# Kernel tuning notes

Hardware: AMD Instinct MI355X
Metric: run time of the kernel (lower is better)

The kernel has to match this reference:

```python
import jax, jax.numpy as jnp
import numpy as np

B, H, S, D = 2, 8, 2048, 64
N_HASHES = 6
EPS = 1e-8


def setup_inputs() -> dict:
    key = jax.random.key(0)
    kq, kk, kv, kr = jax.random.split(key, 4)
    Q = jax.random.normal(kq, (B, H, S, D), dtype=jnp.float32)
    K = jax.random.normal(kk, (B, H, S, D), dtype=jnp.float32)
    V = jax.random.normal(kv, (B, H, S, D), dtype=jnp.float32)
    rotations = jax.random.normal(kr, (H, N_HASHES, D), dtype=jnp.float32)
    return {"Q": Q, "K": K, "V": V, "rotations": rotations}


def _buckets(X, rotations, powers):
    # X: [b,h,l,d] -> integer bucket id per position, [b,h,l]
    Xn = X / (jnp.linalg.norm(X, axis=-1, keepdims=True) + 1e-8)
    bits = jnp.einsum('bhld,hnd->bhln', Xn, rotations) > 0
    return jnp.sum(bits.astype(jnp.int32) * powers, axis=-1)


def reference(Q, K, V, rotations):
    n_hashes = rotations.shape[1]
    d = Q.shape[-1]
    powers = (2 ** jnp.arange(n_hashes)).astype(jnp.int32)
    q_buckets = _buckets(Q, rotations, powers)  # [b,h,sq]
    k_buckets = _buckets(K, rotations, powers)  # [b,h,sk]
    # queries only attend to keys whose full hash code matches exactly
    match = q_buckets[..., :, None] == k_buckets[..., None, :]  # [b,h,sq,sk]
    scores = jnp.einsum('bhqd,bhkd->bhqk', Q, K) / (d ** 0.5)
    row_has = jnp.any(match, axis=-1, keepdims=True)
    masked = jnp.where(match, scores, -jnp.inf)
    m = jnp.max(masked, axis=-1, keepdims=True)
    m = jnp.where(row_has, m, 0.0)  # avoid -inf for empty rows
    e = jnp.where(match, jnp.exp(scores - m), 0.0)
    weights = e / (jnp.sum(e, axis=-1, keepdims=True) + EPS)
    out = jnp.einsum('bhqk,bhkd->bhqd', weights, V)
    return out / n_hashes
```

## Files before the change

kernel.cpp:

```cpp
#include <hip/hip_runtime.h>
#include <math.h>


constexpr int S_LEN = 2048;
constexpr int D = 64;
constexpr int NHASH = 6;
constexpr int BH = 16;
constexpr int NB = 64;
constexpr int QPAD = 4;
constexpr int PADQ = S_LEN + (QPAD - 1) * NB;
constexpr int NGRP = PADQ / QPAD;
constexpr int NBLK = NGRP / 4;
constexpr int GSTRIDE = 37;

__global__ __launch_bounds__(256) void lsh_buckets2(const float* __restrict__ Q,
                                                    const float* __restrict__ K,
                                                    const float* __restrict__ rot,
                                                    int* __restrict__ qb,
                                                    int* __restrict__ kb) {
    const int gw   = (blockIdx.x * 256 + threadIdx.x) >> 6;
    const int lane = threadIdx.x & 63;
    const bool isK = gw >= BH * S_LEN;
    const int wid  = isK ? gw - BH * S_LEN : gw;
    const float* X = isK ? K : Q;
    int* dst       = isK ? kb : qb;
    const int h    = (wid >> 11) & 7;

    const float x  = X[(size_t)wid * D + lane];
    const float* r = rot + (size_t)h * NHASH * D + lane;
    float p0 = x * r[0 * D], p1 = x * r[1 * D], p2 = x * r[2 * D];
    float p3 = x * r[3 * D], p4 = x * r[4 * D], p5 = x * r[5 * D];
#pragma unroll
    for (int off = 32; off >= 1; off >>= 1) {
        p0 += __shfl_xor(p0, off, 64);
        p1 += __shfl_xor(p1, off, 64);
        p2 += __shfl_xor(p2, off, 64);
        p3 += __shfl_xor(p3, off, 64);
        p4 += __shfl_xor(p4, off, 64);
        p5 += __shfl_xor(p5, off, 64);
    }
    int bucket = (p0 > 0.f ? 1 : 0) | (p1 > 0.f ? 2 : 0) | (p2 > 0.f ? 4 : 0) |
                 (p3 > 0.f ? 8 : 0) | (p4 > 0.f ? 16 : 0) | (p5 > 0.f ? 32 : 0);
    if (lane == 0) dst[wid] = bucket;
}

__global__ __launch_bounds__(256) void lsh_sortfuse_bh(const int* __restrict__ qbuckets,
                                                       const int* __restrict__ kbuckets,
                                                       int* __restrict__ q_plist,
                                                       int* __restrict__ k_list) {
    __shared__ int hist[NB];
    __shared__ int cur[NB];
    __shared__ int kst[NB], kcnt[NB];
    __shared__ int qst[NB];
    __shared__ int total;
    const int bh  = blockIdx.x;
    const int tid = threadIdx.x;

    if (tid < NB) hist[tid] = 0;
    __syncthreads();
    int myk[8];
#pragma unroll
    for (int i = 0; i < 8; ++i) {
        myk[i] = kbuckets[bh * S_LEN + i * 256 + tid];
        atomicAdd(&hist[myk[i]], 1);
    }
    __syncthreads();
    if (tid < NB) {
        const int cnt = hist[tid];
        int x = cnt;
#pragma unroll
        for (int off = 1; off < 64; off <<= 1) {
            const int y = __shfl_up(x, off, 64);
            if (tid >= off) x += y;
        }
        kst[tid]  = x - cnt;
        kcnt[tid] = cnt;
        cur[tid]  = x - cnt;
    }
    __syncthreads();
    {
        int* klp = k_list + bh * S_LEN;
#pragma unroll
        for (int i = 0; i < 8; ++i) {
            const int b    = myk[i];
            const int slot = atomicAdd(&cur[b], 1);
            klp[slot] = i * 256 + tid;
        }
    }
    __syncthreads();

    if (tid < NB) hist[tid] = 0;
    __syncthreads();
    int myq[8];
#pragma unroll
    for (int i = 0; i < 8; ++i) {
        myq[i] = qbuckets[bh * S_LEN + i * 256 + tid];
        atomicAdd(&hist[myq[i]], 1);
    }
    __syncthreads();
    if (tid < NB) {
        const int cnt = hist[tid];
        const int v   = (cnt + QPAD - 1) & ~(QPAD - 1);
        int x = v;
#pragma unroll
        for (int off = 1; off < 64; off <<= 1) {
            const int y = __shfl_up(x, off, 64);
            if (tid >= off) x += y;
        }
        qst[tid] = x - v;
        cur[tid] = x - v;
        if (tid == 63) total = x;
    }
    __syncthreads();

    int* qp = q_plist + bh * PADQ;
    if (tid < NB) {
        const int cnt    = hist[tid];
        const int padded = (cnt + QPAD - 1) & ~(QPAD - 1);
        const int sent   = 0xFFFF | (kcnt[tid] << 16);
        for (int t = qst[tid] + cnt; t < qst[tid] + padded; ++t) qp[t] = sent;
    }
    for (int t = total + tid; t < PADQ; t += 256) qp[t] = -1;
#pragma unroll
    for (int i = 0; i < 8; ++i) {
        const int b    = myq[i];
        const int slot = atomicAdd(&cur[b], 1);
        const int pos  = slot & 3;
        int e = i * 256 + tid;
        if (pos == 0)      e |= kst[b] << 16;
        else if (pos == 1) e |= kcnt[b] << 16;
        qp[slot] = e;
    }
}

__global__ __launch_bounds__(256) void lsh_attn_g(const float* __restrict__ Q,
                                                  const float* __restrict__ K,
                                                  const float* __restrict__ V,
                                                  const int* __restrict__ q_plist,
                                                  const int* __restrict__ k_list,
                                                  float* __restrict__ out) {
    __shared__ float wbuf[4][QPAD][64];
    __shared__ int   kbuf[4][64];

    const int wv   = threadIdx.x >> 6;
    const int lane = threadIdx.x & 63;
    const int w    = blockIdx.x;
    const int bh   = (w & 7) + 8 * ((w >> 3) & 1);
    const int gb   = ((w >> 4) * GSTRIDE) % NBLK;
    const int grp  = gb * 4 + wv;

    const int* pl = q_plist + bh * PADQ + 4 * grp;
    const int e0 = __builtin_amdgcn_readfirstlane(pl[0]);
    if ((e0 & 0xFFFF) == 0xFFFF) return;
    const int e1 = __builtin_amdgcn_readfirstlane(pl[1]);
    const int e2 = __builtin_amdgcn_readfirstlane(pl[2]);
    const int e3 = __builtin_amdgcn_readfirstlane(pl[3]);

    const int q0 = e0 & 0xFFFF;
    const int ks = (unsigned)e0 >> 16;
    const int nk = (unsigned)e1 >> 16;
    const int t1 = e1 & 0xFFFF, t2 = e2 & 0xFFFF, t3 = e3 & 0xFFFF;
    const bool v1 = t1 != 0xFFFF, v2 = t2 != 0xFFFF, v3 = t3 != 0xFFFF;
    const int q1 = v1 ? t1 : q0;
    const int q2 = v2 ? t2 : q0;
    const int q3 = v3 ? t3 : q0;

    float* outb = out + (size_t)bh * S_LEN * D;
    if (nk == 0) {
        outb[(size_t)q0 * D + lane] = 0.0f;
        if (v1) outb[(size_t)q1 * D + lane] = 0.0f;
        if (v2) outb[(size_t)q2 * D + lane] = 0.0f;
        if (v3) outb[(size_t)q3 * D + lane] = 0.0f;
        return;
    }

    const int* kl     = k_list + bh * S_LEN + ks;
    const float* Kb   = K + (size_t)bh * S_LEN * D;
    const float* Vb   = V + (size_t)bh * S_LEN * D;
    const float* qr0  = Q + ((size_t)bh * S_LEN + q0) * D;
    const float* qr1  = Q + ((size_t)bh * S_LEN + q1) * D;
    const float* qr2  = Q + ((size_t)bh * S_LEN + q2) * D;
    const float* qr3  = Q + ((size_t)bh * S_LEN + q3) * D;

    float l0 = 0.f, l1 = 0.f, l2 = 0.f, l3 = 0.f;
    float acc0 = 0.f, acc1 = 0.f, acc2 = 0.f, acc3 = 0.f;

    for (int c = 0; c * 64 < nk; ++c) {
        const int cnk  = min(64, nk - c * 64);
        const int kidx = kl[c * 64 + min(lane, cnk - 1)];
        const float* krow = Kb + (size_t)kidx * D;

        float s0 = 0.f, s1 = 0.f, s2 = 0.f, s3 = 0.f;
#pragma unroll
        for (int d4 = 0; d4 < 16; ++d4) {
            const float4 kv = *(const float4*)(krow + d4 * 4);
            const float4 a  = *(const float4*)(qr0 + d4 * 4);
            const float4 b  = *(const float4*)(qr1 + d4 * 4);
            const float4 cq = *(const float4*)(qr2 + d4 * 4);
            const float4 dq = *(const float4*)(qr3 + d4 * 4);
            s0 += a.x * kv.x + a.y * kv.y + a.z * kv.z + a.w * kv.w;
            s1 += b.x * kv.x + b.y * kv.y + b.z * kv.z + b.w * kv.w;
            s2 += cq.x * kv.x + cq.y * kv.y + cq.z * kv.z + cq.w * kv.w;
            s3 += dq.x * kv.x + dq.y * kv.y + dq.z * kv.z + dq.w * kv.w;
        }

        const bool kvalid = lane < cnk;
        const float ea = kvalid ? __expf(s0 * 0.125f) : 0.f;
        const float eb = kvalid ? __expf(s1 * 0.125f) : 0.f;
        const float ec = kvalid ? __expf(s2 * 0.125f) : 0.f;
        const float ed = kvalid ? __expf(s3 * 0.125f) : 0.f;
        l0 += ea; l1 += eb; l2 += ec; l3 += ed;
        wbuf[wv][0][lane] = ea;
        wbuf[wv][1][lane] = eb;
        wbuf[wv][2][lane] = ec;
        wbuf[wv][3][lane] = ed;
        kbuf[wv][lane]    = kidx;

        const int ng = (cnk + 3) >> 2;
        for (int g = 0; g < ng; ++g) {
            const int4   kk = *(const int4*)&kbuf[wv][g * 4];
            const float4 eA = *(const float4*)&wbuf[wv][0][g * 4];
            const float4 eB = *(const float4*)&wbuf[wv][1][g * 4];
            const float4 eC = *(const float4*)&wbuf[wv][2][g * 4];
            const float4 eD = *(const float4*)&wbuf[wv][3][g * 4];
            const float vx = Vb[(size_t)kk.x * D + lane];
            const float vy = Vb[(size_t)kk.y * D + lane];
            const float vz = Vb[(size_t)kk.z * D + lane];
            const float vw = Vb[(size_t)kk.w * D + lane];
            acc0 += eA.x * vx + eA.y * vy + eA.z * vz + eA.w * vw;
            acc1 += eB.x * vx + eB.y * vy + eB.z * vz + eB.w * vw;
            acc2 += eC.x * vx + eC.y * vy + eC.z * vz + eC.w * vw;
            acc3 += eD.x * vx + eD.y * vy + eD.z * vz + eD.w * vw;
        }
    }

#pragma unroll
    for (int off = 32; off >= 1; off >>= 1) {
        l0 += __shfl_xor(l0, off, 64);
        l1 += __shfl_xor(l1, off, 64);
        l2 += __shfl_xor(l2, off, 64);
        l3 += __shfl_xor(l3, off, 64);
    }

    const float inv6 = 1.0f / 6.0f;
    outb[(size_t)q0 * D + lane] = acc0 / (l0 + 1e-8f) * inv6;
    if (v1) outb[(size_t)q1 * D + lane] = acc1 / (l1 + 1e-8f) * inv6;
    if (v2) outb[(size_t)q2 * D + lane] = acc2 / (l2 + 1e-8f) * inv6;
    if (v3) outb[(size_t)q3 * D + lane] = acc3 / (l3 + 1e-8f) * inv6;
}

extern "C" void kernel_launch(void* const* d_in, const int* in_sizes, int n_in,
                              void* d_out, int out_size, void* d_ws, size_t ws_size,
                              hipStream_t stream) {
    const float* Q   = (const float*)d_in[0];
    const float* K   = (const float*)d_in[1];
    const float* V   = (const float*)d_in[2];
    const float* rot = (const float*)d_in[3];
    float* out = (float*)d_out;

    char* ws = (char*)d_ws;
    int* q_buckets = (int*)(ws);
    int* k_buckets = (int*)(ws + 131072);
    int* k_list    = (int*)(ws + 262144);
    int* q_plist   = (int*)(ws + 393216);

    lsh_buckets2<<<2 * BH * S_LEN / 4, 256, 0, stream>>>(Q, K, rot, q_buckets, k_buckets);
    lsh_sortfuse_bh<<<BH, 256, 0, stream>>>(q_buckets, k_buckets, q_plist, k_list);
    lsh_attn_g<<<NBLK * BH, 256, 0, stream>>>(Q, K, V, q_plist, k_list, out);
}
```

Before: 75.88 us.

## Pre-pack bucket-sorted K into transposed float4 layout for coalesced score loads

Adds a kernel that gathers K rows in bucket-sorted key order and writes them as [d/4][slot][4] blocks, so the attention kernel reads K with float4 loads that are contiguous across lanes instead of per-lane scattered row reads. The original attention kernel is kept as a fallback when the workspace is too small. The cost is an extra launch plus a full write and re-read of K (about 4 MB).

After: 72.71 us, median of 2. -4.2%, faster.

```diff
diff --git a/kernel.cpp b/kernel.cpp
--- a/kernel.cpp
+++ b/kernel.cpp
@@ -12,6 +12,7 @@
 constexpr int NGRP = PADQ / QPAD;
 constexpr int NBLK = NGRP / 4;
 constexpr int GSTRIDE = 37;
+constexpr size_t KTP_OFF = 1u << 20;
 
 __global__ __launch_bounds__(256) void lsh_buckets2(const float* __restrict__ Q,
                                                     const float* __restrict__ K,
@@ -133,9 +134,29 @@
     }
 }
 
-__global__ __launch_bounds__(256) void lsh_attn_g(const float* __restrict__ Q,
-                                                  const float* __restrict__ K,
+__global__ __launch_bounds__(256) void lsh_kpack(const float* __restrict__ K,
+                                                 const int* __restrict__ k_list,
+                                                 float* __restrict__ Ktp) {
+    const int gw   = (blockIdx.x * 256 + threadIdx.x) >> 6;
+    const int lane = threadIdx.x & 63;
+    const int bh   = gw >> 9;
+    const int s0   = (gw & 511) * 4;
+    const float* Kb = K + (size_t)bh * S_LEN * D;
+    const int* kl   = k_list + bh * S_LEN;
+    float* kt       = Ktp + (size_t)bh * 16 * S_LEN * 4;
+    const int dblk  = lane >> 2, dj = lane & 3;
+#pragma unroll
+    for (int j = 0; j < 4; ++j) {
+        const int slot = s0 + j;
+        const int kidx = kl[slot];
+        const float v  = Kb[(size_t)kidx * D + lane];
+        kt[((size_t)dblk * S_LEN + slot) * 4 + dj] = v;
+    }
+}
+
+__global__ __launch_bounds__(256) void lsh_attn_p(const float* __restrict__ Q,
                                                   const float* __restrict__ V,
+                                                  const float* __restrict__ Ktp,
                                                   const int* __restrict__ q_plist,
                                                   const int* __restrict__ k_list,
                                                   float* __restrict__ out) {
@@ -175,7 +196,7 @@
     }
 
     const int* kl     = k_list + bh * S_LEN + ks;
-    const float* Kb   = K + (size_t)bh * S_LEN * D;
+    const float* ktb  = Ktp + (size_t)bh * 16 * S_LEN * 4;
     const float* Vb   = V + (size_t)bh * S_LEN * D;
     const float* qr0  = Q + ((size_t)bh * S_LEN + q0) * D;
     const float* qr1  = Q + ((size_t)bh * S_LEN + q1) * D;
@@ -187,13 +208,14 @@
 
     for (int c = 0; c * 64 < nk; ++c) {
         const int cnk  = min(64, nk - c * 64);
-        const int kidx = kl[c * 64 + min(lane, cnk - 1)];
-        const float* krow = Kb + (size_t)kidx * D;
+        const int cl   = min(lane, cnk - 1);
+        const int kidx = kl[c * 64 + cl];
+        const int slot = ks + c * 64 + cl;
 
         float s0 = 0.f, s1 = 0.f, s2 = 0.f, s3 = 0.f;
 #pragma unroll
         for (int d4 = 0; d4 < 16; ++d4) {
-            const float4 kv = *(const float4*)(krow + d4 * 4);
+            const float4 kv = *(const float4*)(ktb + ((size_t)d4 * S_LEN + slot) * 4);
             const float4 a  = *(const float4*)(qr0 + d4 * 4);
             const float4 b  = *(const float4*)(qr1 + d4 * 4);
             const float4 cq = *(const float4*)(qr2 + d4 * 4);
@@ -249,6 +271,122 @@
     if (v3) outb[(size_t)q3 * D + lane] = acc3 / (l3 + 1e-8f) * inv6;
 }
 
+__global__ __launch_bounds__(256) void lsh_attn_g(const float* __restrict__ Q,
+                                                  const float* __restrict__ K,
+                                                  const float* __restrict__ V,
+                                                  const int* __restrict__ q_plist,
+                                                  const int* __restrict__ k_list,
+                                                  float* __restrict__ out) {
+    __shared__ float wbuf[4][QPAD][64];
+    __shared__ int   kbuf[4][64];
+
+    const int wv   = threadIdx.x >> 6;
+    const int lane = threadIdx.x & 63;
+    const int w    = blockIdx.x;
+    const int bh   = (w & 7) + 8 * ((w >> 3) & 1);
+    const int gb   = ((w >> 4) * GSTRIDE) % NBLK;
+    const int grp  = gb * 4 + wv;
+
+    const int* pl = q_plist + bh * PADQ + 4 * grp;
+    const int e0 = __builtin_amdgcn_readfirstlane(pl[0]);
+    if ((e0 & 0xFFFF) == 0xFFFF) return;
+    const int e1 = __builtin_amdgcn_readfirstlane(pl[1]);
+    const int e2 = __builtin_amdgcn_readfirstlane(pl[2]);
+    const int e3 = __builtin_amdgcn_readfirstlane(pl[3]);
+
+    const int q0 = e0 & 0xFFFF;
+    const int ks = (unsigned)e0 >> 16;
+    const int nk = (unsigned)e1 >> 16;
+    const int t1 = e1 & 0xFFFF, t2 = e2 & 0xFFFF, t3 = e3 & 0xFFFF;
+    const bool v1 = t1 != 0xFFFF, v2 = t2 != 0xFFFF, v3 = t3 != 0xFFFF;
+    const int q1 = v1 ? t1 : q0;
+    const int q2 = v2 ? t2 : q0;
+    const int q3 = v3 ? t3 : q0;
+
+    float* outb = out + (size_t)bh * S_LEN * D;
+    if (nk == 0) {
+        outb[(size_t)q0 * D + lane] = 0.0f;
+        if (v1) outb[(size_t)q1 * D + lane] = 0.0f;
+        if (v2) outb[(size_t)q2 * D + lane] = 0.0f;
+        if (v3) outb[(size_t)q3 * D + lane] = 0.0f;
+        return;
+    }
+
+    const int* kl     = k_list + bh * S_LEN + ks;
+    const float* Kb   = K + (size_t)bh * S_LEN * D;
+    const float* Vb   = V + (size_t)bh * S_LEN * D;
+    const float* qr0  = Q + ((size_t)bh * S_LEN + q0) * D;
+    const float* qr1  = Q + ((size_t)bh * S_LEN + q1) * D;
+    const float* qr2  = Q + ((size_t)bh * S_LEN + q2) * D;
+    const float* qr3  = Q + ((size_t)bh * S_LEN + q3) * D;
+
+    float l0 = 0.f, l1 = 0.f, l2 = 0.f, l3 = 0.f;
+    float acc0 = 0.f, acc1 = 0.f, acc2 = 0.f, acc3 = 0.f;
+
+    for (int c = 0; c * 64 < nk; ++c) {
+        const int cnk  = min(64, nk - c * 64);
+        const int kidx = kl[c * 64 + min(lane, cnk - 1)];
+        const float* krow = Kb + (size_t)kidx * D;
+
+        float s0 = 0.f, s1 = 0.f, s2 = 0.f, s3 = 0.f;
+#pragma unroll
+        for (int d4 = 0; d4 < 16; ++d4) {
+            const float4 kv = *(const float4*)(krow + d4 * 4);
+            const float4 a  = *(const float4*)(qr0 + d4 * 4);
+            const float4 b  = *(const float4*)(qr1 + d4 * 4);
+            const float4 cq = *(const float4*)(qr2 + d4 * 4);
+            const float4 dq = *(const float4*)(qr3 + d4 * 4);
+            s0 += a.x * kv.x + a.y * kv.y + a.z * kv.z + a.w * kv.w;
+            s1 += b.x * kv.x + b.y * kv.y + b.z * kv.z + b.w * kv.w;
+            s2 += cq.x * kv.x + cq.y * kv.y + cq.z * kv.z + cq.w * kv.w;
+            s3 += dq.x * kv.x + dq.y * kv.y + dq.z * kv.z + dq.w * kv.w;
+        }
+
+        const bool kvalid = lane < cnk;
+        const float ea = kvalid ? __expf(s0 * 0.125f) : 0.f;
+        const float eb = kvalid ? __expf(s1 * 0.125f) : 0.f;
+        const float ec = kvalid ? __expf(s2 * 0.125f) : 0.f;
+        const float ed = kvalid ? __expf(s3 * 0.125f) : 0.f;
+        l0 += ea; l1 += eb; l2 += ec; l3 += ed;
+        wbuf[wv][0][lane] = ea;
+        wbuf[wv][1][lane] = eb;
+        wbuf[wv][2][lane] = ec;
+        wbuf[wv][3][lane] = ed;
+        kbuf[wv][lane]    = kidx;
+
+        const int ng = (cnk + 3) >> 2;
+        for (int g = 0; g < ng; ++g) {
+            const int4   kk = *(const int4*)&kbuf[wv][g * 4];
+            const float4 eA = *(const float4*)&wbuf[wv][0][g * 4];
+            const float4 eB = *(const float4*)&wbuf[wv][1][g * 4];
+            const float4 eC = *(const float4*)&wbuf[wv][2][g * 4];
+            const float4 eD = *(const float4*)&wbuf[wv][3][g * 4];
+            const float vx = Vb[(size_t)kk.x * D + lane];
+            const float vy = Vb[(size_t)kk.y * D + lane];
+            const float vz = Vb[(size_t)kk.z * D + lane];
+            const float vw = Vb[(size_t)kk.w * D + lane];
+            acc0 += eA.x * vx + eA.y * vy + eA.z * vz + eA.w * vw;
+            acc1 += eB.x * vx + eB.y * vy + eB.z * vz + eB.w * vw;
+            acc2 += eC.x * vx + eC.y * vy + eC.z * vz + eC.w * vw;
+            acc3 += eD.x * vx + eD.y * vy + eD.z * vz + eD.w * vw;
+        }
+    }
+
+#pragma unroll
+    for (int off = 32; off >= 1; off >>= 1) {
+        l0 += __shfl_xor(l0, off, 64);
+        l1 += __shfl_xor(l1, off, 64);
+        l2 += __shfl_xor(l2, off, 64);
+        l3 += __shfl_xor(l3, off, 64);
+    }
+
+    const float inv6 = 1.0f / 6.0f;
+    outb[(size_t)q0 * D + lane] = acc0 / (l0 + 1e-8f) * inv6;
+    if (v1) outb[(size_t)q1 * D + lane] = acc1 / (l1 + 1e-8f) * inv6;
+    if (v2) outb[(size_t)q2 * D + lane] = acc2 / (l2 + 1e-8f) * inv6;
+    if (v3) outb[(size_t)q3 * D + lane] = acc3 / (l3 + 1e-8f) * inv6;
+}
+
 extern "C" void kernel_launch(void* const* d_in, const int* in_sizes, int n_in,
                               void* d_out, int out_size, void* d_ws, size_t ws_size,
                               hipStream_t stream) {
@@ -263,8 +401,17 @@
     int* k_buckets = (int*)(ws + 131072);
     int* k_list    = (int*)(ws + 262144);
     int* q_plist   = (int*)(ws + 393216);
+    float* Ktp     = (float*)(ws + KTP_OFF);
+
+    const size_t ktp_bytes = (size_t)BH * 16 * S_LEN * 4 * sizeof(float);
+    const bool packed = ws_size >= KTP_OFF + ktp_bytes;
 
     lsh_buckets2<<<2 * BH * S_LEN / 4, 256, 0, stream>>>(Q, K, rot, q_buckets, k_buckets);
     lsh_sortfuse_bh<<<BH, 256, 0, stream>>>(q_buckets, k_buckets, q_plist, k_list);
-    lsh_attn_g<<<NBLK * BH, 256, 0, stream>>>(Q, K, V, q_plist, k_list, out);
-}
+    if (packed) {
+        lsh_kpack<<<BH * S_LEN / 16, 256, 0, stream>>>(K, k_list, Ktp);
+        lsh_attn_p<<<NBLK * BH, 256, 0, stream>>>(Q, V, Ktp, q_plist, k_list, out);
+    } else {
+        lsh_attn_g<<<NBLK * BH, 256, 0, stream>>>(Q, K, V, q_plist, k_list, out);
+    }
+}
```
